# Performance work log

Measured on AMD Instinct MI355X. Metric: run time of the kernel, lower is better.

The kernel has to match this reference:

```python
import jax, jax.numpy as jnp
import numpy as np

INPUT_SIZE = 64 * 64 * 10  # 40960
H1, H2, H3 = 256, 32, 32
BATCH = 2048


def _linear_init(key, out_f, in_f):
    # torch nn.Linear default init: U(-1/sqrt(in_f), 1/sqrt(in_f))
    kw, kb = jax.random.split(key)
    bound = 1.0 / np.sqrt(in_f)
    W = jax.random.uniform(kw, (out_f, in_f), jnp.float32, -bound, bound)
    b = jax.random.uniform(kb, (out_f,), jnp.float32, -bound, bound)
    return W, b


def setup_inputs() -> dict:
    key = jax.random.key(0)
    ks = jax.random.split(key, 7)
    input_player = jax.random.uniform(ks[0], (BATCH, INPUT_SIZE), jnp.float32)
    input_opponent = jax.random.uniform(ks[1], (BATCH, INPUT_SIZE), jnp.float32)
    W1p, b1p = _linear_init(ks[2], H1, INPUT_SIZE)
    W1o, b1o = _linear_init(ks[3], H1, INPUT_SIZE)
    W2, b2 = _linear_init(ks[4], H2, 2 * H1)
    W3, b3 = _linear_init(ks[5], H3, H2)
    Wo, bo = _linear_init(ks[6], 1, H3)
    return {
        "input_player": input_player, "input_opponent": input_opponent,
        "W1p": W1p, "b1p": b1p, "W1o": W1o, "b1o": b1o,
        "W2": W2, "b2": b2, "W3": W3, "b3": b3, "Wo": Wo, "bo": bo,
    }


def _crelu(x):
    # ReLU followed by clamp(0, 1) == clipped ReLU
    return jnp.clip(x, 0.0, 1.0)


def reference(input_player, input_opponent, W1p, b1p, W1o, b1o, W2, b2, W3, b3, Wo, bo):
    # Feature transformer (sparse-in-practice 40960 -> 256 per perspective)
    acc_p = _crelu(input_player @ W1p.T + b1p)    # [B, 256]
    acc_o = _crelu(input_opponent @ W1o.T + b1o)  # [B, 256]
    combined = jnp.concatenate([acc_p, acc_o], axis=-1)  # [B, 512]
    h = _crelu(combined @ W2.T + b2)  # [B, 32]
    h = _crelu(h @ W3.T + b3)         # [B, 32]
    out = _crelu(h @ Wo.T + bo)       # [B, 1]
    return out
```

## Files before the change

kernel.cpp:

```cpp
#include <hip/hip_runtime.h>

#define K_DIM 40960
#define NFEAT 256
#define BATCH 2048

typedef _Float16 f16;
typedef _Float16 f16x8 __attribute__((ext_vector_type(8)));
typedef _Float16 f16x4 __attribute__((ext_vector_type(4)));
typedef float f32x4 __attribute__((ext_vector_type(4)));

__global__ __launch_bounds__(256) void convert_w(
    const float* __restrict__ w1p, const float* __restrict__ w1o,
    f16* __restrict__ w16p, f16* __restrict__ w16o) {
  const long N4 = (long)NFEAT * K_DIM / 4;
  long stride = (long)gridDim.x * blockDim.x;
  for (long i = (long)blockIdx.x * blockDim.x + threadIdx.x; i < 2 * N4; i += stride) {
    const float4* src;
    f16* dst;
    long idx;
    if (i < N4) { src = (const float4*)w1p; dst = w16p; idx = i; }
    else        { src = (const float4*)w1o; dst = w16o; idx = i - N4; }
    float4 v = src[idx];
    f16x4 h;
    h.x = (f16)v.x; h.y = (f16)v.y; h.z = (f16)v.z; h.w = (f16)v.w;
    *(f16x4*)(dst + idx * 4) = h;
  }
}

__global__ __launch_bounds__(256, 2) void ft_gemm(
    const float* __restrict__ Ap, const float* __restrict__ Ao,
    const f16* __restrict__ W16p, const f16* __restrict__ W16o,
    const float* __restrict__ W32p, const float* __restrict__ W32o,
    int use_w16, int S, float* __restrict__ partials) {
  __shared__ f16 Ash[64 * 72];
  __shared__ f16 Wsh[256 * 64];

  int b = blockIdx.x;
  int persp = b & 1;
  int t = b >> 1;
  int s = t % S;
  int mt = t / S;
  int mbase = mt * 64;

  const float* A = persp ? Ao : Ap;
  const f16* W16 = persp ? W16o : W16p;
  const float* W32 = persp ? W32o : W32p;

  int tid = threadIdx.x;
  int lane = tid & 63;
  int wv = tid >> 6;
  int mrow = lane & 15;
  int kq = lane >> 4;

  f32x4 acc[4][4];
#pragma unroll
  for (int rt = 0; rt < 4; ++rt)
#pragma unroll
    for (int ct = 0; ct < 4; ++ct)
      acc[rt][ct] = (f32x4){0.f, 0.f, 0.f, 0.f};

  const int krange = K_DIM / S;
  const int kstart = s * krange;

  for (int k0 = kstart; k0 < kstart + krange; k0 += 64) {
#pragma unroll
    for (int i = 0; i < 4; ++i) {
      int f = i * 256 + tid;
      int row = f >> 4;
      int cb = f & 15;
      float4 v = *(const float4*)(A + (size_t)(mbase + row) * K_DIM + k0 + cb * 4);
      f16x4 h;
      h.x = (f16)v.x; h.y = (f16)v.y; h.z = (f16)v.z; h.w = (f16)v.w;
      *(f16x4*)&Ash[row * 72 + cb * 4] = h;
    }
    if (use_w16) {
#pragma unroll
      for (int i = 0; i < 8; ++i) {
        int f = i * 256 + tid;
        int rl = f >> 3;
        int kbs = f & 7;
        int kbg = kbs ^ (rl & 7);
        f16x8 v = *(const f16x8*)(W16 + (size_t)rl * K_DIM + k0 + kbg * 8);
        *(f16x8*)&Wsh[rl * 64 + kbs * 8] = v;
      }
    } else {
#pragma unroll
      for (int i = 0; i < 8; ++i) {
        int f = i * 256 + tid;
        int rl = f >> 3;
        int kbs = f & 7;
        int kbg = kbs ^ (rl & 7);
        const float* src = W32 + (size_t)rl * K_DIM + k0 + kbg * 8;
        float4 v0 = *(const float4*)(src);
        float4 v1 = *(const float4*)(src + 4);
        f16x8 h;
        h[0] = (f16)v0.x; h[1] = (f16)v0.y; h[2] = (f16)v0.z; h[3] = (f16)v0.w;
        h[4] = (f16)v1.x; h[5] = (f16)v1.y; h[6] = (f16)v1.z; h[7] = (f16)v1.w;
        *(f16x8*)&Wsh[rl * 64 + kbs * 8] = h;
      }
    }
    __syncthreads();

#pragma unroll
    for (int ks = 0; ks < 2; ++ks) {
      f16x8 afrag[4], bfrag[4];
#pragma unroll
      for (int rt = 0; rt < 4; ++rt)
        afrag[rt] = *(const f16x8*)&Ash[(rt * 16 + mrow) * 72 + ks * 32 + kq * 8];
#pragma unroll
      for (int ct = 0; ct < 4; ++ct) {
        int rown = wv * 64 + ct * 16 + mrow;
        int kb = ks * 4 + kq;
        int kbp = kb ^ (rown & 7);
        bfrag[ct] = *(const f16x8*)&Wsh[rown * 64 + kbp * 8];
      }
#pragma unroll
      for (int rt = 0; rt < 4; ++rt)
#pragma unroll
        for (int ct = 0; ct < 4; ++ct)
          acc[rt][ct] = __builtin_amdgcn_mfma_f32_16x16x32_f16(
              afrag[rt], bfrag[ct], acc[rt][ct], 0, 0, 0);
    }
    __syncthreads();
  }

  float* pp = partials + ((size_t)persp * S + s) * ((size_t)BATCH * NFEAT);
#pragma unroll
  for (int rt = 0; rt < 4; ++rt)
#pragma unroll
    for (int ct = 0; ct < 4; ++ct) {
      int col = wv * 64 + ct * 16 + mrow;
#pragma unroll
      for (int i = 0; i < 4; ++i) {
        int row = mbase + rt * 16 + kq * 4 + i;
        pp[(size_t)row * NFEAT + col] = acc[rt][ct][i];
      }
    }
}

__global__ __launch_bounds__(256) void reduce_bias(
    const float* __restrict__ partials, const float* __restrict__ b1p,
    const float* __restrict__ b1o, int S, float* __restrict__ combined) {
  int idx = blockIdx.x * blockDim.x + threadIdx.x;
  int r = idx >> 9;
  int c = idx & 511;
  int persp = c >> 8;
  int n = c & 255;
  float sum = persp ? b1o[n] : b1p[n];
  const float* p = partials + (size_t)persp * S * BATCH * NFEAT + (size_t)r * NFEAT + n;
  for (int s = 0; s < S; ++s) sum += p[(size_t)s * BATCH * NFEAT];
  sum = fminf(fmaxf(sum, 0.f), 1.f);
  combined[(size_t)r * 512 + c] = sum;
}

__global__ __launch_bounds__(256) void mlp(
    const float* __restrict__ combined, const float* __restrict__ W2,
    const float* __restrict__ b2, const float* __restrict__ W3,
    const float* __restrict__ b3, const float* __restrict__ Wo,
    const float* __restrict__ bo, float* __restrict__ out) {
  __shared__ float H1s[8][33];
  __shared__ float H2s[8][33];
  int tid = threadIdx.x;
  int lr = tid >> 5;
  int j = tid & 31;
  int r = blockIdx.x * 8 + lr;

  const float* crow = combined + (size_t)r * 512;
  const float* w2r = W2 + j * 512;
  float acc = b2[j];
#pragma unroll 8
  for (int k = 0; k < 512; ++k) acc += crow[k] * w2r[k];
  H1s[lr][j] = fminf(fmaxf(acc, 0.f), 1.f);
  __syncthreads();

  acc = b3[j];
  const float* w3r = W3 + j * 32;
#pragma unroll
  for (int k = 0; k < 32; ++k) acc += H1s[lr][k] * w3r[k];
  H2s[lr][j] = fminf(fmaxf(acc, 0.f), 1.f);
  __syncthreads();

  if (j == 0) {
    float o = bo[0];
#pragma unroll
    for (int k = 0; k < 32; ++k) o += H2s[lr][k] * Wo[k];
    out[r] = fminf(fmaxf(o, 0.f), 1.f);
  }
}

extern "C" void kernel_launch(void* const* d_in, const int* in_sizes, int n_in,
                              void* d_out, int out_size, void* d_ws, size_t ws_size,
                              hipStream_t stream) {
  const float* Ap  = (const float*)d_in[0];
  const float* Ao  = (const float*)d_in[1];
  const float* W1p = (const float*)d_in[2];
  const float* b1p = (const float*)d_in[3];
  const float* W1o = (const float*)d_in[4];
  const float* b1o = (const float*)d_in[5];
  const float* W2  = (const float*)d_in[6];
  const float* b2  = (const float*)d_in[7];
  const float* W3  = (const float*)d_in[8];
  const float* b3  = (const float*)d_in[9];
  const float* Wo  = (const float*)d_in[10];
  const float* bo  = (const float*)d_in[11];
  float* out = (float*)d_out;

  const size_t W16B = 2UL * NFEAT * K_DIM * 2;
  const size_t COMB = (size_t)BATCH * 512 * 4;
  auto need = [&](int s, int w16) {
    return (w16 ? W16B : 0) + (size_t)s * 2 * BATCH * NFEAT * 4 + COMB;
  };

  int S = 8, use_w16 = 1;
  while (S > 1 && need(S, 1) > ws_size) S >>= 1;
  if (need(S, 1) > ws_size) {
    use_w16 = 0;
    S = 8;
    while (S > 1 && need(S, 0) > ws_size) S >>= 1;
  }

  char* ws = (char*)d_ws;
  f16* W16p = (f16*)ws;
  f16* W16o = W16p + (size_t)NFEAT * K_DIM;
  float* partials = (float*)(ws + (use_w16 ? W16B : 0));
  float* combined = partials + (size_t)S * 2 * BATCH * NFEAT;

  if (use_w16)
    convert_w<<<1024, 256, 0, stream>>>(W1p, W1o, W16p, W16o);

  int grid = (BATCH / 64) * S * 2;
  ft_gemm<<<grid, 256, 0, stream>>>(Ap, Ao, W16p, W16o, W1p, W1o, use_w16, S, partials);

  reduce_bias<<<(BATCH * 512) / 256, 256, 0, stream>>>(partials, b1p, b1o, S, combined);

  mlp<<<BATCH / 8, 256, 0, stream>>>(combined, W2, b2, W3, b3, Wo, bo, out);
}
```

Baseline: 803.0 us.

## Prefetch tiles into registers, use 512-thread blocks, store fp16 split-K partials

```diff
diff --git a/kernel.cpp b/kernel.cpp
--- a/kernel.cpp
+++ b/kernel.cpp
@@ -7,6 +7,7 @@
 typedef _Float16 f16;
 typedef _Float16 f16x8 __attribute__((ext_vector_type(8)));
 typedef _Float16 f16x4 __attribute__((ext_vector_type(4)));
+typedef _Float16 f16x2 __attribute__((ext_vector_type(2)));
 typedef float f32x4 __attribute__((ext_vector_type(4)));
 
 __global__ __launch_bounds__(256) void convert_w(
@@ -22,135 +23,143 @@
     else        { src = (const float4*)w1o; dst = w16o; idx = i - N4; }
     float4 v = src[idx];
     f16x4 h;
-    h.x = (f16)v.x; h.y = (f16)v.y; h.z = (f16)v.z; h.w = (f16)v.w;
+    h[0] = (f16)v.x; h[1] = (f16)v.y; h[2] = (f16)v.z; h[3] = (f16)v.w;
     *(f16x4*)(dst + idx * 4) = h;
   }
 }
 
-__global__ __launch_bounds__(256, 2) void ft_gemm(
+__global__ __launch_bounds__(512, 4) void ft_gemm(
     const float* __restrict__ Ap, const float* __restrict__ Ao,
     const f16* __restrict__ W16p, const f16* __restrict__ W16o,
-    const float* __restrict__ W32p, const float* __restrict__ W32o,
-    int use_w16, int S, float* __restrict__ partials) {
-  __shared__ f16 Ash[64 * 72];
+    int S, f16* __restrict__ partials) {
+  __shared__ f16 Ash[64 * 64];
   __shared__ f16 Wsh[256 * 64];
 
-  int b = blockIdx.x;
-  int persp = b & 1;
-  int t = b >> 1;
-  int s = t % S;
-  int mt = t / S;
-  int mbase = mt * 64;
+  const int b = blockIdx.x;
+  const int G = 2 * S;
+  const int g = b % G;
+  const int mt = b / G;
+  const int persp = g & 1;
+  const int s = g >> 1;
+  const int mbase = mt * 64;
 
   const float* A = persp ? Ao : Ap;
   const f16* W16 = persp ? W16o : W16p;
-  const float* W32 = persp ? W32o : W32p;
-
-  int tid = threadIdx.x;
-  int lane = tid & 63;
-  int wv = tid >> 6;
-  int mrow = lane & 15;
-  int kq = lane >> 4;
-
-  f32x4 acc[4][4];
+
+  const int tid = threadIdx.x;
+  const int lane = tid & 63;
+  const int wv = tid >> 6;
+  const int mrow = lane & 15;
+  const int kq = lane >> 4;
+
+  f32x4 acc[4][2];
 #pragma unroll
   for (int rt = 0; rt < 4; ++rt)
 #pragma unroll
-    for (int ct = 0; ct < 4; ++ct)
+    for (int ct = 0; ct < 2; ++ct)
       acc[rt][ct] = (f32x4){0.f, 0.f, 0.f, 0.f};
 
   const int krange = K_DIM / S;
   const int kstart = s * krange;
-
-  for (int k0 = kstart; k0 < kstart + krange; k0 += 64) {
-#pragma unroll
-    for (int i = 0; i < 4; ++i) {
-      int f = i * 256 + tid;
-      int row = f >> 4;
-      int cb = f & 15;
-      float4 v = *(const float4*)(A + (size_t)(mbase + row) * K_DIM + k0 + cb * 4);
+  const int kend = kstart + krange;
+
+  int a_row[2], a_cb[2];
+#pragma unroll
+  for (int i = 0; i < 2; ++i) { int f = i * 512 + tid; a_row[i] = f >> 4; a_cb[i] = f & 15; }
+  int w_rl[4], w_kbs[4], w_kbg[4];
+#pragma unroll
+  for (int i = 0; i < 4; ++i) {
+    int f = i * 512 + tid; w_rl[i] = f >> 3; w_kbs[i] = f & 7; w_kbg[i] = w_kbs[i] ^ (w_rl[i] & 7);
+  }
+
+  float4 pa[2];
+  f16x8 pw[4];
+#pragma unroll
+  for (int i = 0; i < 2; ++i)
+    pa[i] = *(const float4*)(A + (size_t)(mbase + a_row[i]) * K_DIM + kstart + a_cb[i] * 4);
+#pragma unroll
+  for (int i = 0; i < 4; ++i)
+    pw[i] = *(const f16x8*)(W16 + (size_t)w_rl[i] * K_DIM + kstart + w_kbg[i] * 8);
+
+  for (int k0 = kstart; k0 < kend; k0 += 64) {
+#pragma unroll
+    for (int i = 0; i < 2; ++i) {
+      int row = a_row[i], cb = a_cb[i];
+      int slot = (cb >> 1) ^ (row & 7);
       f16x4 h;
-      h.x = (f16)v.x; h.y = (f16)v.y; h.z = (f16)v.z; h.w = (f16)v.w;
-      *(f16x4*)&Ash[row * 72 + cb * 4] = h;
+      h[0] = (f16)pa[i].x; h[1] = (f16)pa[i].y; h[2] = (f16)pa[i].z; h[3] = (f16)pa[i].w;
+      *(f16x4*)&Ash[row * 64 + slot * 8 + (cb & 1) * 4] = h;
     }
-    if (use_w16) {
-#pragma unroll
-      for (int i = 0; i < 8; ++i) {
-        int f = i * 256 + tid;
-        int rl = f >> 3;
-        int kbs = f & 7;
-        int kbg = kbs ^ (rl & 7);
-        f16x8 v = *(const f16x8*)(W16 + (size_t)rl * K_DIM + k0 + kbg * 8);
-        *(f16x8*)&Wsh[rl * 64 + kbs * 8] = v;
+#pragma unroll
+    for (int i = 0; i < 4; ++i)
+      *(f16x8*)&Wsh[w_rl[i] * 64 + w_kbs[i] * 8] = pw[i];
+    __syncthreads();
+
+    const int kn = (k0 + 64 < kend) ? (k0 + 64) : kstart;
+#pragma unroll
+    for (int i = 0; i < 2; ++i)
+      pa[i] = *(const float4*)(A + (size_t)(mbase + a_row[i]) * K_DIM + kn + a_cb[i] * 4);
+#pragma unroll
+    for (int i = 0; i < 4; ++i)
+      pw[i] = *(const f16x8*)(W16 + (size_t)w_rl[i] * K_DIM + kn + w_kbg[i] * 8);
+
+#pragma unroll
+    for (int ks = 0; ks < 2; ++ks) {
+      const int kb = ks * 4 + kq;
+      f16x8 af[4], bf[2];
+#pragma unroll
+      for (int rt = 0; rt < 4; ++rt) {
+        int row = rt * 16 + mrow;
+        af[rt] = *(const f16x8*)&Ash[row * 64 + (kb ^ (row & 7)) * 8];
       }
-    } else {
-#pragma unroll
-      for (int i = 0; i < 8; ++i) {
-        int f = i * 256 + tid;
-        int rl = f >> 3;
-        int kbs = f & 7;
-        int kbg = kbs ^ (rl & 7);
-        const float* src = W32 + (size_t)rl * K_DIM + k0 + kbg * 8;
-        float4 v0 = *(const float4*)(src);
-        float4 v1 = *(const float4*)(src + 4);
-        f16x8 h;
-        h[0] = (f16)v0.x; h[1] = (f16)v0.y; h[2] = (f16)v0.z; h[3] = (f16)v0.w;
-        h[4] = (f16)v1.x; h[5] = (f16)v1.y; h[6] = (f16)v1.z; h[7] = (f16)v1.w;
-        *(f16x8*)&Wsh[rl * 64 + kbs * 8] = h;
+#pragma unroll
+      for (int ct = 0; ct < 2; ++ct) {
+        int rown = (wv * 2 + ct) * 16 + mrow;
+        bf[ct] = *(const f16x8*)&Wsh[rown * 64 + (kb ^ (rown & 7)) * 8];
+      }
+#pragma unroll
+      for (int rt = 0; rt < 4; ++rt)
+#pragma unroll
+        for (int ct = 0; ct < 2; ++ct)
+          acc[rt][ct] = __builtin_amdgcn_mfma_f32_16x16x32_f16(af[rt], bf[ct], acc[rt][ct], 0, 0, 0);
+    }
+    __syncthreads();
+  }
+
+  f16* pp = partials + (size_t)g * ((size_t)BATCH * NFEAT);
+#pragma unroll
+  for (int rt = 0; rt < 4; ++rt)
+#pragma unroll
+    for (int ct = 0; ct < 2; ++ct) {
+      int col = (wv * 2 + ct) * 16 + mrow;
+#pragma unroll
+      for (int i = 0; i < 4; ++i) {
+        int row = mbase + rt * 16 + kq * 4 + i;
+        pp[(size_t)row * NFEAT + col] = (f16)acc[rt][ct][i];
       }
     }
-    __syncthreads();
-
-#pragma unroll
-    for (int ks = 0; ks < 2; ++ks) {
-      f16x8 afrag[4], bfrag[4];
-#pragma unroll
-      for (int rt = 0; rt < 4; ++rt)
-        afrag[rt] = *(const f16x8*)&Ash[(rt * 16 + mrow) * 72 + ks * 32 + kq * 8];
-#pragma unroll
-      for (int ct = 0; ct < 4; ++ct) {
-        int rown = wv * 64 + ct * 16 + mrow;
-        int kb = ks * 4 + kq;
-        int kbp = kb ^ (rown & 7);
-        bfrag[ct] = *(const f16x8*)&Wsh[rown * 64 + kbp * 8];
-      }
-#pragma unroll
-      for (int rt = 0; rt < 4; ++rt)
-#pragma unroll
-        for (int ct = 0; ct < 4; ++ct)
-          acc[rt][ct] = __builtin_amdgcn_mfma_f32_16x16x32_f16(
-              afrag[rt], bfrag[ct], acc[rt][ct], 0, 0, 0);
-    }
-    __syncthreads();
-  }
-
-  float* pp = partials + ((size_t)persp * S + s) * ((size_t)BATCH * NFEAT);
-#pragma unroll
-  for (int rt = 0; rt < 4; ++rt)
-#pragma unroll
-    for (int ct = 0; ct < 4; ++ct) {
-      int col = wv * 64 + ct * 16 + mrow;
-#pragma unroll
-      for (int i = 0; i < 4; ++i) {
-        int row = mbase + rt * 16 + kq * 4 + i;
-        pp[(size_t)row * NFEAT + col] = acc[rt][ct][i];
-      }
-    }
 }
 
 __global__ __launch_bounds__(256) void reduce_bias(
-    const float* __restrict__ partials, const float* __restrict__ b1p,
+    const f16* __restrict__ partials, const float* __restrict__ b1p,
     const float* __restrict__ b1o, int S, float* __restrict__ combined) {
-  int idx = blockIdx.x * blockDim.x + threadIdx.x;
-  int r = idx >> 9;
-  int c = idx & 511;
-  int persp = c >> 8;
-  int n = c & 255;
-  float sum = persp ? b1o[n] : b1p[n];
-  const float* p = partials + (size_t)persp * S * BATCH * NFEAT + (size_t)r * NFEAT + n;
-  for (int s = 0; s < S; ++s) sum += p[(size_t)s * BATCH * NFEAT];
-  sum = fminf(fmaxf(sum, 0.f), 1.f);
-  combined[(size_t)r * 512 + c] = sum;
+  int idx = blockIdx.x * 256 + threadIdx.x;
+  int r = idx >> 8;
+  int c2 = idx & 255;
+  int persp = c2 >> 7;
+  int n = (c2 & 127) * 2;
+  const float* bias = persp ? b1o : b1p;
+  float s0 = bias[n], s1 = bias[n + 1];
+#pragma unroll 4
+  for (int s = 0; s < S; ++s) {
+    f16x2 v = *(const f16x2*)(partials + ((size_t)(s * 2 + persp)) * BATCH * NFEAT +
+                              (size_t)r * NFEAT + n);
+    s0 += (float)v[0]; s1 += (float)v[1];
+  }
+  s0 = fminf(fmaxf(s0, 0.f), 1.f);
+  s1 = fminf(fmaxf(s1, 0.f), 1.f);
+  float2 o; o.x = s0; o.y = s1;
+  *(float2*)(combined + (size_t)r * 512 + persp * 256 + n) = o;
 }
 
 __global__ __launch_bounds__(256) void mlp(
@@ -158,18 +167,27 @@
     const float* __restrict__ b2, const float* __restrict__ W3,
     const float* __restrict__ b3, const float* __restrict__ Wo,
     const float* __restrict__ bo, float* __restrict__ out) {
+  __shared__ f16 W2T[512 * 33];
   __shared__ float H1s[8][33];
   __shared__ float H2s[8][33];
   int tid = threadIdx.x;
+#pragma unroll
+  for (int i = 0; i < 64; ++i) {
+    int idx = i * 256 + tid;
+    int j = idx >> 9;
+    int k = idx & 511;
+    W2T[k * 33 + j] = (f16)W2[idx];
+  }
+  __syncthreads();
+
   int lr = tid >> 5;
   int j = tid & 31;
   int r = blockIdx.x * 8 + lr;
 
   const float* crow = combined + (size_t)r * 512;
-  const float* w2r = W2 + j * 512;
   float acc = b2[j];
 #pragma unroll 8
-  for (int k = 0; k < 512; ++k) acc += crow[k] * w2r[k];
+  for (int k = 0; k < 512; ++k) acc += crow[k] * (float)W2T[k * 33 + j];
   H1s[lr][j] = fminf(fmaxf(acc, 0.f), 1.f);
   __syncthreads();
 
@@ -207,31 +225,25 @@
 
   const size_t W16B = 2UL * NFEAT * K_DIM * 2;
   const size_t COMB = (size_t)BATCH * 512 * 4;
-  auto need = [&](int s, int w16) {
-    return (w16 ? W16B : 0) + (size_t)s * 2 * BATCH * NFEAT * 4 + COMB;
+  auto need = [&](int s) {
+    return W16B + (size_t)s * 2 * BATCH * NFEAT * 2 + COMB;
   };
 
-  int S = 8, use_w16 = 1;
-  while (S > 1 && need(S, 1) > ws_size) S >>= 1;
-  if (need(S, 1) > ws_size) {
-    use_w16 = 0;
-    S = 8;
-    while (S > 1 && need(S, 0) > ws_size) S >>= 1;
-  }
+  int S = 16;
+  while (S > 1 && need(S) > ws_size) S >>= 1;
 
   char* ws = (char*)d_ws;
   f16* W16p = (f16*)ws;
   f16* W16o = W16p + (size_t)NFEAT * K_DIM;
-  float* partials = (float*)(ws + (use_w16 ? W16B : 0));
-  float* combined = partials + (size_t)S * 2 * BATCH * NFEAT;
-
-  if (use_w16)
-    convert_w<<<1024, 256, 0, stream>>>(W1p, W1o, W16p, W16o);
+  f16* partials = (f16*)(ws + W16B);
+  float* combined = (float*)(ws + W16B + (size_t)S * 2 * BATCH * NFEAT * 2);
+
+  convert_w<<<1024, 256, 0, stream>>>(W1p, W1o, W16p, W16o);
 
   int grid = (BATCH / 64) * S * 2;
-  ft_gemm<<<grid, 256, 0, stream>>>(Ap, Ao, W16p, W16o, W1p, W1o, use_w16, S, partials);
-
-  reduce_bias<<<(BATCH * 512) / 256, 256, 0, stream>>>(partials, b1p, b1o, S, combined);
+  ft_gemm<<<grid, 512, 0, stream>>>(Ap, Ao, W16p, W16o, S, partials);
+
+  reduce_bias<<<(BATCH * 256) / 256, 256, 0, stream>>>(partials, b1p, b1o, S, combined);
 
   mlp<<<BATCH / 8, 256, 0, stream>>>(combined, W2, b2, W3, b3, Wo, bo, out);
 }
```

Result: faster. 776.4 us (-3.3%).
